# Kernel optimization log

Hardware: AMD Instinct MI355X
Metric: run time of the kernel (lower is better)

Reference implementation:

```python
import jax, jax.numpy as jnp
import numpy as np

N_NODES = 50000
N_EDGES = 500000
IN_FEAT = 128
OUT_FEAT = 128
N_REL = 16


def setup_inputs() -> dict:
    key = jax.random.key(0)
    k1, k2, k3, k4 = jax.random.split(key, 4)
    entity_embeddings = jax.random.normal(k1, (N_NODES, IN_FEAT), dtype=jnp.float32)
    # xavier_uniform over (in, out) fan per relation slice
    limit = (6.0 / (IN_FEAT + OUT_FEAT)) ** 0.5
    weight = jax.random.uniform(k2, (N_REL, IN_FEAT, OUT_FEAT), dtype=jnp.float32,
                                minval=-limit, maxval=limit)
    edge_index = jax.random.randint(k3, (2, N_EDGES), 0, N_NODES, dtype=jnp.int64)
    edge_type = jax.random.randint(k4, (N_EDGES,), 0, N_REL, dtype=jnp.int64)
    return {"entity_embeddings": entity_embeddings, "weight": weight,
            "edge_index": edge_index, "edge_type": edge_type}


def reference(entity_embeddings, weight, edge_index, edge_type):
    # RGCN message passing: for each edge e with relation r:
    #   msg_e = x[src_e] @ W[r];  out[tgt_e] += msg_e;  out = relu(out)
    # Vectorized: transform every node by every relation once (R*N*in*out flops),
    # then gather the (relation, src) slice per edge and scatter-add to tgt.
    # This avoids gathering a per-edge (E, in, out) weight tensor.
    num_entities = entity_embeddings.shape[0]
    src = edge_index[0]
    tgt = edge_index[1]
    transformed = jnp.einsum('ni,rio->rno', entity_embeddings, weight)  # (R, N, O)
    msg = transformed[edge_type, src]                                   # (E, O)
    messages = jax.ops.segment_sum(msg, tgt, num_segments=num_entities)  # (N, O)
    # Dropout is identity in eval mode; reference omits it (deterministic baseline).
    return jax.nn.relu(messages)
```

## Files before the change

### kernel.cpp

```cpp
#include <hip/hip_runtime.h>
#include <hip/hip_bf16.h>

typedef __attribute__((ext_vector_type(8))) __bf16 bf16x8;
typedef __attribute__((ext_vector_type(4))) __bf16 bf16x4;
typedef __attribute__((ext_vector_type(2))) __bf16 bf16x2;
typedef __attribute__((ext_vector_type(4))) float f32x4;

#define IN_FEAT 128
#define OUT_FEAT 128
#define N_REL 16
#define TILE_M 64
#define GEMM_GRID 1024

__global__ void cvtX_kernel(const float* __restrict__ x, __bf16* __restrict__ xb, int n) {
    int i = (blockIdx.x * blockDim.x + threadIdx.x) * 4;
    if (i < n) {
        float4 v = *(const float4*)(x + i);
        bf16x4 o = { (__bf16)v.x, (__bf16)v.y, (__bf16)v.z, (__bf16)v.w };
        *(bf16x4*)(xb + i) = o;
    }
}

__global__ __launch_bounds__(256) void cvtW2_kernel(const float* __restrict__ w,
                                                    __bf16* __restrict__ wt) {
    __shared__ __bf16 tile[32 * 136];
    int r = blockIdx.x >> 2;
    int n0 = (blockIdx.x & 3) * 32;
    const float* W = w + (size_t)r * IN_FEAT * OUT_FEAT;
    __bf16* T = wt + (size_t)r * IN_FEAT * OUT_FEAT;
    int t = threadIdx.x;
    #pragma unroll
    for (int it = 0; it < 16; ++it) {
        int idx = t + it * 256;
        int k = idx >> 5, dn = idx & 31;
        tile[dn * 136 + k] = (__bf16)W[k * OUT_FEAT + n0 + dn];
    }
    __syncthreads();
    #pragma unroll
    for (int it = 0; it < 2; ++it) {
        int idx = t + it * 256;
        int n = idx >> 4, c = idx & 15;
        bf16x8 v = *(const bf16x8*)(&tile[n * 136 + c * 8]);
        *(bf16x8*)(T + (size_t)(n0 + n) * IN_FEAT + c * 8) = v;
    }
}

__global__ void hist_kernel(const int* __restrict__ etype, const int* __restrict__ etgt,
                            int n, int* __restrict__ cnt_rel, int* __restrict__ cnt_tgt) {
    __shared__ int h[N_REL];
    if (threadIdx.x < N_REL) h[threadIdx.x] = 0;
    __syncthreads();
    for (int i = blockIdx.x * blockDim.x + threadIdx.x; i < n; i += gridDim.x * blockDim.x) {
        atomicAdd(&h[etype[i]], 1);
        if (cnt_tgt) atomicAdd(&cnt_tgt[etgt[i]], 1);
    }
    __syncthreads();
    if (threadIdx.x < N_REL) atomicAdd(&cnt_rel[threadIdx.x], h[threadIdx.x]);
}

__global__ void prefix_kernel(const int* __restrict__ cnt, int* __restrict__ meta) {
    if (threadIdx.x == 0) {
        int off = 0, toff = 0;
        for (int r = 0; r < N_REL; ++r) {
            meta[r] = off; meta[32 + r] = toff; meta[64 + r] = off;
            off += cnt[r];
            toff += (cnt[r] + TILE_M - 1) / TILE_M;
        }
        meta[16] = off; meta[48] = toff;
    }
}

__global__ void scanA_kernel(const int* __restrict__ cnt, int n, int* __restrict__ partial) {
    __shared__ int s[256];
    int i = blockIdx.x * 256 + threadIdx.x;
    s[threadIdx.x] = (i < n) ? cnt[i] : 0;
    __syncthreads();
    for (int off = 128; off > 0; off >>= 1) {
        if (threadIdx.x < off) s[threadIdx.x] += s[threadIdx.x + off];
        __syncthreads();
    }
    if (threadIdx.x == 0) partial[blockIdx.x] = s[0];
}
__global__ void scanBP_kernel(int* __restrict__ partial, int nchunks,
                              const int* __restrict__ cnt_rel, int* __restrict__ meta) {
    __shared__ int s[256];
    int t = threadIdx.x;
    int v = (t < nchunks) ? partial[t] : 0;
    s[t] = v;
    __syncthreads();
    for (int off = 1; off < 256; off <<= 1) {
        int x = (t >= off) ? s[t - off] : 0;
        __syncthreads();
        s[t] += x;
        __syncthreads();
    }
    if (t < nchunks) partial[t] = s[t] - v;
    if (t == 0) {
        int off = 0, toff = 0;
        for (int r = 0; r < N_REL; ++r) {
            meta[r] = off; meta[32 + r] = toff; meta[64 + r] = off;
            off += cnt_rel[r];
            toff += (cnt_rel[r] + TILE_M - 1) / TILE_M;
        }
        meta[16] = off; meta[48] = toff;
    }
}
__global__ void scanC_kernel(const int* __restrict__ cnt, int n, const int* __restrict__ partial,
                             int* __restrict__ base, int* __restrict__ cursor) {
    __shared__ int s[256];
    int t = threadIdx.x, i = blockIdx.x * 256 + t;
    int v = (i < n) ? cnt[i] : 0;
    s[t] = v;
    __syncthreads();
    for (int off = 1; off < 256; off <<= 1) {
        int x = (t >= off) ? s[t - off] : 0;
        __syncthreads();
        s[t] += x;
        __syncthreads();
    }
    int b = partial[blockIdx.x] + s[t] - v;
    if (i < n) { base[i] = b; cursor[i] = b; }
}

#define SCATTER_EPT 2
#define SCATTER_CHUNK (256 * SCATTER_EPT)
__global__ __launch_bounds__(256) void scatter_slot_kernel(
        const int* __restrict__ esrc, const int* __restrict__ etgt,
        const int* __restrict__ etype, int n,
        int* __restrict__ cursor_rel, int* __restrict__ cursor_tgt,
        int* __restrict__ bsrc, int* __restrict__ bslot) {
    __shared__ int lcnt[N_REL];
    __shared__ int lbase[N_REL];
    int t = threadIdx.x;
    if (t < N_REL) lcnt[t] = 0;
    __syncthreads();
    int base = blockIdx.x * SCATTER_CHUNK;
    int rj[SCATTER_EPT], offj[SCATTER_EPT];
    #pragma unroll
    for (int j = 0; j < SCATTER_EPT; ++j) {
        int i = base + j * 256 + t;
        if (i < n) {
            int r = etype[i];
            rj[j] = r;
            offj[j] = atomicAdd(&lcnt[r], 1);
        } else rj[j] = -1;
    }
    __syncthreads();
    if (t < N_REL) lbase[t] = atomicAdd(&cursor_rel[t], lcnt[t]);
    __syncthreads();
    #pragma unroll
    for (int j = 0; j < SCATTER_EPT; ++j) {
        if (rj[j] >= 0) {
            int i = base + j * 256 + t;
            int p = lbase[rj[j]] + offj[j];
            bsrc[p] = esrc[i];
            bslot[p] = atomicAdd(&cursor_tgt[etgt[i]], 1);
        }
    }
}

__global__ __launch_bounds__(256) void scatter_kernel(
        const int* __restrict__ esrc, const int* __restrict__ etgt,
        const int* __restrict__ etype, int n,
        int* __restrict__ cursor,
        int* __restrict__ bsrc, int* __restrict__ btgt) {
    __shared__ int lcnt[N_REL];
    __shared__ int lbase[N_REL];
    int t = threadIdx.x;
    if (t < N_REL) lcnt[t] = 0;
    __syncthreads();
    int base = blockIdx.x * SCATTER_CHUNK;
    int rj[SCATTER_EPT], offj[SCATTER_EPT];
    #pragma unroll
    for (int j = 0; j < SCATTER_EPT; ++j) {
        int i = base + j * 256 + t;
        if (i < n) {
            int r = etype[i];
            rj[j] = r;
            offj[j] = atomicAdd(&lcnt[r], 1);
        } else rj[j] = -1;
    }
    __syncthreads();
    if (t < N_REL) lbase[t] = atomicAdd(&cursor[t], lcnt[t]);
    __syncthreads();
    #pragma unroll
    for (int j = 0; j < SCATTER_EPT; ++j) {
        if (rj[j] >= 0) {
            int i = base + j * 256 + t;
            int p = lbase[rj[j]] + offj[j];
            bsrc[p] = esrc[i];
            btgt[p] = etgt[i];
        }
    }
}

__global__ __launch_bounds__(256, 3) void gemm_msg4_kernel(
    const __bf16* __restrict__ Xb,
    const __bf16* __restrict__ Wt,
    const int* __restrict__ bsrc, const int* __restrict__ bslot,
    const int* __restrict__ meta,
    __bf16* __restrict__ msg) {
    __shared__ __align__(16) __bf16 Bs[OUT_FEAT * 128];
    __shared__ __align__(16) __bf16 As[TILE_M * 128];
    __shared__ int s_slot[TILE_M];

    const int* rel_off = meta;
    const int* tile_pre = meta + 32;
    int T = tile_pre[16];
    int chunk = (T + GEMM_GRID - 1) / GEMM_GRID;
    int t0 = blockIdx.x * chunk;
    if (t0 >= T) return;
    int t1 = min(T, t0 + chunk);

    int tid = threadIdx.x;
    int wave = tid >> 6, lane = tid & 63;
    int q = lane >> 4, ln = lane & 15;
    uint4* BsV = (uint4*)Bs;
    uint4* AsV = (uint4*)As;
    const bf16x8* AsF = (const bf16x8*)As;
    const bf16x8* BsF = (const bf16x8*)Bs;

    int arow = tid & 63;
    int acb  = tid >> 6;

    int cur_rel = -1;
    uint4 apf[4];
    int spf = 0;
    {
        int r = 0; while (t0 >= tile_pre[r + 1]) ++r;
        int row_start = rel_off[r] + (t0 - tile_pre[r]) * TILE_M;
        int m_valid = min(TILE_M, rel_off[r + 1] - row_start);
        int src = bsrc[row_start + min(arow, m_valid - 1)];
        const uint4* xr = (const uint4*)(Xb + (size_t)src * IN_FEAT);
        #pragma unroll
        for (int i = 0; i < 4; ++i) apf[i] = xr[acb + 4 * i];
        if (tid < TILE_M) spf = (tid < m_valid) ? bslot[row_start + tid] : -1;
    }

    for (int tt = t0; tt < t1; ++tt) {
        int r = 0; while (tt >= tile_pre[r + 1]) ++r;
        __syncthreads();
        if (r != cur_rel) {
            cur_rel = r;
            const __bf16* wsrc = Wt + (size_t)r * IN_FEAT * OUT_FEAT;
            #pragma unroll
            for (int i = 0; i < 8; ++i) {
                int cid = tid + i * 256;
                int row = cid >> 4, c = cid & 15;
                int feat = (row & 15) * 8 + (row >> 4);
                uint4 v = *(const uint4*)(wsrc + (size_t)feat * IN_FEAT + c * 8);
                BsV[row * 16 + (c ^ (row & 15))] = v;
            }
        }
        #pragma unroll
        for (int i = 0; i < 4; ++i) {
            int c = acb + 4 * i;
            AsV[arow * 16 + (c ^ (arow & 15))] = apf[i];
        }
        if (tid < TILE_M) s_slot[tid] = spf;

        if (tt + 1 < t1) {
            int rn = 0; while (tt + 1 >= tile_pre[rn + 1]) ++rn;
            int row_start = rel_off[rn] + (tt + 1 - tile_pre[rn]) * TILE_M;
            int m_valid = min(TILE_M, rel_off[rn + 1] - row_start);
            int src = bsrc[row_start + min(arow, m_valid - 1)];
            const uint4* xr = (const uint4*)(Xb + (size_t)src * IN_FEAT);
            #pragma unroll
            for (int i = 0; i < 4; ++i) apf[i] = xr[acb + 4 * i];
            if (tid < TILE_M) spf = (tid < m_valid) ? bslot[row_start + tid] : -1;
        }
        __syncthreads();

        f32x4 acc[8];
        f32x4 z = { 0.f, 0.f, 0.f, 0.f };
        #pragma unroll
        for (int nf = 0; nf < 8; ++nf) acc[nf] = z;

        int myrow = wave * 16 + ln;
        #pragma unroll
        for (int kk = 0; kk < 4; ++kk) {
            bf16x8 a = AsF[myrow * 16 + ((kk * 4 + q) ^ ln)];
            #pragma unroll
            for (int nf = 0; nf < 8; ++nf) {
                bf16x8 b = BsF[(nf * 16 + ln) * 16 + ((kk * 4 + q) ^ ln)];
                acc[nf] = __builtin_amdgcn_mfma_f32_16x16x32_bf16(a, b, acc[nf], 0, 0, 0);
            }
        }

        #pragma unroll
        for (int reg = 0; reg < 4; ++reg) {
            int row = wave * 16 + q * 4 + reg;
            int slot = s_slot[row];
            if (slot >= 0) {
                bf16x8 o = { (__bf16)acc[0][reg], (__bf16)acc[1][reg],
                             (__bf16)acc[2][reg], (__bf16)acc[3][reg],
                             (__bf16)acc[4][reg], (__bf16)acc[5][reg],
                             (__bf16)acc[6][reg], (__bf16)acc[7][reg] };
                *(bf16x8*)(msg + (size_t)slot * OUT_FEAT + ln * 8) = o;
            }
        }
    }
}

__global__ __launch_bounds__(256) void segsum2_kernel(
        const __bf16* __restrict__ msg, const int* __restrict__ base,
        int nnodes, int ntot, float* __restrict__ out) {
    int n = blockIdx.x * 4 + (threadIdx.x >> 6);
    if (n >= nnodes) return;
    int l = threadIdx.x & 63;
    int half = l >> 5, cl = l & 31;
    int s0 = base[n];
    int s1 = (n == nnodes - 1) ? ntot : base[n + 1];
    float4 a = { 0.f, 0.f, 0.f, 0.f };
    int s = s0;
    for (; s + 2 <= s1; s += 2) {
        bf16x4 m = *(const bf16x4*)(msg + (size_t)(s + half) * OUT_FEAT + cl * 4);
        a.x += (float)m[0]; a.y += (float)m[1]; a.z += (float)m[2]; a.w += (float)m[3];
    }
    if (s < s1 && half == 0) {
        bf16x4 m = *(const bf16x4*)(msg + (size_t)s * OUT_FEAT + cl * 4);
        a.x += (float)m[0]; a.y += (float)m[1]; a.z += (float)m[2]; a.w += (float)m[3];
    }
    a.x += __shfl_xor(a.x, 32, 64);
    a.y += __shfl_xor(a.y, 32, 64);
    a.z += __shfl_xor(a.z, 32, 64);
    a.w += __shfl_xor(a.w, 32, 64);
    if (half == 0) {
        float4 o = { fmaxf(a.x, 0.f), fmaxf(a.y, 0.f), fmaxf(a.z, 0.f), fmaxf(a.w, 0.f) };
        *(float4*)(out + (size_t)n * OUT_FEAT + cl * 4) = o;
    }
}

#define LDA 136
__global__ __launch_bounds__(256) void gemm_scatter_kernel(
    const __bf16* __restrict__ Xb, const __bf16* __restrict__ Wt,
    const int* __restrict__ bsrc, const int* __restrict__ btgt,
    const int* __restrict__ meta, float* __restrict__ out) {
    __shared__ __align__(16) __bf16 As2[TILE_M * LDA];
    __shared__ __align__(16) __bf16 Bs2[OUT_FEAT * LDA];
    __shared__ int s_tgt[TILE_M];
    int bid = blockIdx.x;
    const int* rel_off = meta;
    const int* tile_pre = meta + 32;
    if (bid >= tile_pre[16]) return;
    int rel = 0;
    while (bid >= tile_pre[rel + 1]) rel++;
    int tile = bid - tile_pre[rel];
    int row_start = rel_off[rel] + tile * TILE_M;
    int m_valid = min(TILE_M, rel_off[rel + 1] - row_start);
    int t = threadIdx.x;
    {
        const __bf16* src = Wt + rel * IN_FEAT * OUT_FEAT;
        #pragma unroll
        for (int i = 0; i < 8; ++i) {
            int cid = t + i * 256;
            int n = cid >> 4, c = cid & 15;
            uint4 v = *(const uint4*)(src + n * IN_FEAT + c * 8);
            *(uint4*)(&Bs2[n * LDA + c * 8]) = v;
        }
    }
    {
        #pragma unroll
        for (int i = 0; i < 4; ++i) {
            int cid = t + i * 256;
            int r = cid >> 4, c = cid & 15;
            int srcn = (r < m_valid) ? bsrc[row_start + r] : 0;
            uint4 v = *(const uint4*)(Xb + srcn * IN_FEAT + c * 8);
            *(uint4*)(&As2[r * LDA + c * 8]) = v;
        }
        if (t < TILE_M) s_tgt[t] = (t < m_valid) ? btgt[row_start + t] : -1;
    }
    __syncthreads();
    int wave = t >> 6, lane = t & 63;
    int q = lane >> 4, ln = lane & 15;
    f32x4 acc[8];
    f32x4 z = { 0.f, 0.f, 0.f, 0.f };
    #pragma unroll
    for (int nf = 0; nf < 8; ++nf) acc[nf] = z;
    #pragma unroll
    for (int kk = 0; kk < 4; ++kk) {
        bf16x8 a = *(const bf16x8*)(&As2[(wave * 16 + ln) * LDA + kk * 32 + q * 8]);
        #pragma unroll
        for (int nf = 0; nf < 8; ++nf) {
            bf16x8 b = *(const bf16x8*)(&Bs2[(nf * 16 + ln) * LDA + kk * 32 + q * 8]);
            acc[nf] = __builtin_amdgcn_mfma_f32_16x16x32_bf16(a, b, acc[nf], 0, 0, 0);
        }
    }
    #pragma unroll
    for (int reg = 0; reg < 4; ++reg) {
        int r = wave * 16 + q * 4 + reg;
        int tgt = s_tgt[r];
        if (tgt >= 0) {
            float* orow = out + (size_t)tgt * OUT_FEAT + ln;
            #pragma unroll
            for (int nf = 0; nf < 8; ++nf)
                unsafeAtomicAdd(orow + nf * 16, acc[nf][reg]);
        }
    }
}

__global__ void relu_kernel(float* __restrict__ out, int n) {
    int i = (blockIdx.x * blockDim.x + threadIdx.x) * 4;
    if (i < n) {
        float4 v = *(float4*)(out + i);
        v.x = fmaxf(v.x, 0.f); v.y = fmaxf(v.y, 0.f);
        v.z = fmaxf(v.z, 0.f); v.w = fmaxf(v.w, 0.f);
        *(float4*)(out + i) = v;
    }
}

extern "C" void kernel_launch(void* const* d_in, const int* in_sizes, int n_in,
                              void* d_out, int out_size, void* d_ws, size_t ws_size,
                              hipStream_t stream) {
    const float* x = (const float*)d_in[0];
    const float* w = (const float*)d_in[1];
    const int* eidx = (const int*)d_in[2];
    const int* etype = (const int*)d_in[3];
    const int E = in_sizes[3];
    const int nX = in_sizes[0];
    const int N = out_size / OUT_FEAT;
    const int* esrc = eidx;
    const int* etgt = eidx + E;
    float* out = (float*)d_out;

    char* ws = (char*)d_ws;
    size_t off = 0;
    auto alloc = [&](size_t sz) { size_t o = off; off = (off + sz + 255) & ~(size_t)255; return o; };
    size_t off_Xb   = alloc((size_t)nX * 2);
    size_t off_Wt   = alloc((size_t)N_REL * IN_FEAT * OUT_FEAT * 2);
    size_t off_cnt  = alloc(64);
    size_t off_meta = alloc(512);
    size_t off_bsrc = alloc((size_t)E * 4);
    size_t off_bsl  = alloc((size_t)E * 4);
    size_t off_ctgt = alloc((size_t)(N + 16) * 4);
    size_t off_cur  = alloc((size_t)N * 4);
    size_t off_base = alloc((size_t)N * 4);
    size_t off_part = alloc(1024);
    size_t off_msg  = alloc((size_t)E * OUT_FEAT * 2);
    bool big = (ws_size >= off);

    __bf16* Xb = (__bf16*)(ws + off_Xb);
    __bf16* Wt = (__bf16*)(ws + off_Wt);
    int* meta  = (int*)(ws + off_meta);
    int* bsrc  = (int*)(ws + off_bsrc);
    int* bsl   = (int*)(ws + off_bsl);

    cvtX_kernel<<<(nX / 4 + 255) / 256, 256, 0, stream>>>(x, Xb, nX);
    cvtW2_kernel<<<64, 256, 0, stream>>>(w, Wt);

    int scatter_blocks = (E + SCATTER_CHUNK - 1) / SCATTER_CHUNK;

    if (big) {
        int* cnt_tgt = (int*)(ws + off_ctgt);
        int* cnt_rel = cnt_tgt + N;
        int* cursor  = (int*)(ws + off_cur);
        int* base    = (int*)(ws + off_base);
        int* partial = (int*)(ws + off_part);
        __bf16* msg  = (__bf16*)(ws + off_msg);
        int nchunks = (N + 255) / 256;

        hipMemsetAsync(cnt_tgt, 0, (size_t)(N + 16) * 4, stream);
        hist_kernel<<<1024, 256, 0, stream>>>(etype, etgt, E, cnt_rel, cnt_tgt);
        scanA_kernel<<<nchunks, 256, 0, stream>>>(cnt_tgt, N, partial);
        scanBP_kernel<<<1, 256, 0, stream>>>(partial, nchunks, cnt_rel, meta);
        scanC_kernel<<<nchunks, 256, 0, stream>>>(cnt_tgt, N, partial, base, cursor);
        scatter_slot_kernel<<<scatter_blocks, 256, 0, stream>>>(
            esrc, etgt, etype, E, meta + 64, cursor, bsrc, bsl);
        gemm_msg4_kernel<<<GEMM_GRID, 256, 0, stream>>>(Xb, Wt, bsrc, bsl, meta, msg);
        segsum2_kernel<<<(N + 3) / 4, 256, 0, stream>>>(msg, base, N, E, out);
    } else {
        int* cnt = (int*)(ws + off_cnt);
        hipMemsetAsync(cnt, 0, 64, stream);
        hipMemsetAsync(out, 0, (size_t)out_size * 4, stream);
        hist_kernel<<<1024, 256, 0, stream>>>(etype, etgt, E, cnt, nullptr);
        prefix_kernel<<<1, 64, 0, stream>>>(cnt, meta);
        scatter_kernel<<<scatter_blocks, 256, 0, stream>>>(
            esrc, etgt, etype, E, meta + 64, bsrc, bsl);
        int max_tiles = (E + TILE_M - 1) / TILE_M + N_REL;
        gemm_scatter_kernel<<<max_tiles, 256, 0, stream>>>(Xb, Wt, bsrc, bsl, meta, out);
        relu_kernel<<<(out_size / 4 + 255) / 256, 256, 0, stream>>>(out, out_size);
    }
}
```

Before: 256.0 us.

## Fuse weight conversion into histogram kernel and convert X inside GEMM tiles

Merges the weight transpose/convert with the edge histogram into one prep kernel, drops the separate X-to-bf16 conversion pass in the main path, and has the GEMM read fp32 node features directly and convert them while staging each tile. The GEMM moves from a persistent 1024-block grid with register prefetch to one block per tile, with no occupancy hint in launch bounds. This removes two launches and a full write and re-read of X, but doubles gather bytes per edge row and loses the prefetch overlap.

```diff
diff --git a/kernel.cpp b/kernel.cpp
--- a/kernel.cpp
+++ b/kernel.cpp
@@ -10,7 +10,6 @@
 #define OUT_FEAT 128
 #define N_REL 16
 #define TILE_M 64
-#define GEMM_GRID 1024
 
 __global__ void cvtX_kernel(const float* __restrict__ x, __bf16* __restrict__ xb, int n) {
     int i = (blockIdx.x * blockDim.x + threadIdx.x) * 4;
@@ -21,43 +20,54 @@
     }
 }
 
-__global__ __launch_bounds__(256) void cvtW2_kernel(const float* __restrict__ w,
-                                                    __bf16* __restrict__ wt) {
+__global__ __launch_bounds__(256) void prep_kernel(
+        const float* __restrict__ w, __bf16* __restrict__ wt,
+        const int* __restrict__ etype, const int* __restrict__ etgt, int n,
+        int* __restrict__ cnt_rel, int* __restrict__ cnt_tgt) {
     __shared__ __bf16 tile[32 * 136];
-    int r = blockIdx.x >> 2;
-    int n0 = (blockIdx.x & 3) * 32;
-    const float* W = w + (size_t)r * IN_FEAT * OUT_FEAT;
-    __bf16* T = wt + (size_t)r * IN_FEAT * OUT_FEAT;
+    __shared__ int h[N_REL];
     int t = threadIdx.x;
-    #pragma unroll
-    for (int it = 0; it < 16; ++it) {
-        int idx = t + it * 256;
-        int k = idx >> 5, dn = idx & 31;
-        tile[dn * 136 + k] = (__bf16)W[k * OUT_FEAT + n0 + dn];
-    }
-    __syncthreads();
-    #pragma unroll
-    for (int it = 0; it < 2; ++it) {
-        int idx = t + it * 256;
-        int n = idx >> 4, c = idx & 15;
-        bf16x8 v = *(const bf16x8*)(&tile[n * 136 + c * 8]);
-        *(bf16x8*)(T + (size_t)(n0 + n) * IN_FEAT + c * 8) = v;
-    }
-}
-
-__global__ void hist_kernel(const int* __restrict__ etype, const int* __restrict__ etgt,
-                            int n, int* __restrict__ cnt_rel, int* __restrict__ cnt_tgt) {
+    if (blockIdx.x < 64) {
+        int r = blockIdx.x >> 2;
+        int n0 = (blockIdx.x & 3) * 32;
+        const float* W = w + (size_t)r * IN_FEAT * OUT_FEAT;
+        __bf16* T = wt + (size_t)r * IN_FEAT * OUT_FEAT;
+        #pragma unroll
+        for (int it = 0; it < 16; ++it) {
+            int idx = t + it * 256;
+            int k = idx >> 5, dn = idx & 31;
+            tile[dn * 136 + k] = (__bf16)W[k * OUT_FEAT + n0 + dn];
+        }
+        __syncthreads();
+        #pragma unroll
+        for (int it = 0; it < 2; ++it) {
+            int idx = t + it * 256;
+            int nn = idx >> 4, c = idx & 15;
+            bf16x8 v = *(const bf16x8*)(&tile[nn * 136 + c * 8]);
+            *(bf16x8*)(T + (size_t)(n0 + nn) * IN_FEAT + c * 8) = v;
+        }
+    } else {
+        if (t < N_REL) h[t] = 0;
+        __syncthreads();
+        int stride = (gridDim.x - 64) * blockDim.x;
+        for (int i = (blockIdx.x - 64) * blockDim.x + t; i < n; i += stride) {
+            atomicAdd(&h[etype[i]], 1);
+            atomicAdd(&cnt_tgt[etgt[i]], 1);
+        }
+        __syncthreads();
+        if (t < N_REL) atomicAdd(&cnt_rel[t], h[t]);
+    }
+}
+
+__global__ void hist_kernel(const int* __restrict__ etype, int n, int* __restrict__ cnt_rel) {
     __shared__ int h[N_REL];
     if (threadIdx.x < N_REL) h[threadIdx.x] = 0;
     __syncthreads();
-    for (int i = blockIdx.x * blockDim.x + threadIdx.x; i < n; i += gridDim.x * blockDim.x) {
+    for (int i = blockIdx.x * blockDim.x + threadIdx.x; i < n; i += gridDim.x * blockDim.x)
         atomicAdd(&h[etype[i]], 1);
-        if (cnt_tgt) atomicAdd(&cnt_tgt[etgt[i]], 1);
-    }
     __syncthreads();
     if (threadIdx.x < N_REL) atomicAdd(&cnt_rel[threadIdx.x], h[threadIdx.x]);
 }
-
 __global__ void prefix_kernel(const int* __restrict__ cnt, int* __restrict__ meta) {
     if (threadIdx.x == 0) {
         int off = 0, toff = 0;
@@ -194,8 +204,8 @@
     }
 }
 
-__global__ __launch_bounds__(256, 3) void gemm_msg4_kernel(
-    const __bf16* __restrict__ Xb,
+__global__ __launch_bounds__(256) void gemm_msg5_kernel(
+    const float* __restrict__ X,
     const __bf16* __restrict__ Wt,
     const int* __restrict__ bsrc, const int* __restrict__ bslot,
     const int* __restrict__ meta,
@@ -204,100 +214,78 @@
     __shared__ __align__(16) __bf16 As[TILE_M * 128];
     __shared__ int s_slot[TILE_M];
 
+    int bid = blockIdx.x;
     const int* rel_off = meta;
     const int* tile_pre = meta + 32;
-    int T = tile_pre[16];
-    int chunk = (T + GEMM_GRID - 1) / GEMM_GRID;
-    int t0 = blockIdx.x * chunk;
-    if (t0 >= T) return;
-    int t1 = min(T, t0 + chunk);
+    if (bid >= tile_pre[16]) return;
+    int rel = 0;
+    while (bid >= tile_pre[rel + 1]) rel++;
+    int tile = bid - tile_pre[rel];
+    int row_start = rel_off[rel] + tile * TILE_M;
+    int m_valid = min(TILE_M, rel_off[rel + 1] - row_start);
 
     int tid = threadIdx.x;
+    uint4* BsV = (uint4*)Bs;
+    bf16x8* AsV = (bf16x8*)As;
+    const bf16x8* AsF = (const bf16x8*)As;
+    const bf16x8* BsF = (const bf16x8*)Bs;
+
+    {
+        const __bf16* wsrc = Wt + (size_t)rel * IN_FEAT * OUT_FEAT;
+        #pragma unroll
+        for (int i = 0; i < 8; ++i) {
+            int cid = tid + i * 256;
+            int row = cid >> 4, c = cid & 15;
+            int feat = (row & 15) * 8 + (row >> 4);
+            uint4 v = *(const uint4*)(wsrc + (size_t)feat * IN_FEAT + c * 8);
+            BsV[row * 16 + (c ^ (row & 15))] = v;
+        }
+    }
+    {
+        #pragma unroll
+        for (int i = 0; i < 4; ++i) {
+            int cid = tid + i * 256;
+            int r = cid >> 4, c = cid & 15;
+            int srcn = (r < m_valid) ? bsrc[row_start + r] : 0;
+            const float4* xr = (const float4*)(X + (size_t)srcn * IN_FEAT + c * 8);
+            float4 f0 = xr[0], f1 = xr[1];
+            bf16x8 o = { (__bf16)f0.x, (__bf16)f0.y, (__bf16)f0.z, (__bf16)f0.w,
+                         (__bf16)f1.x, (__bf16)f1.y, (__bf16)f1.z, (__bf16)f1.w };
+            AsV[r * 16 + (c ^ (r & 15))] = o;
+        }
+        if (tid < TILE_M) s_slot[tid] = (tid < m_valid) ? bslot[row_start + tid] : -1;
+    }
+    __syncthreads();
+
     int wave = tid >> 6, lane = tid & 63;
     int q = lane >> 4, ln = lane & 15;
-    uint4* BsV = (uint4*)Bs;
-    uint4* AsV = (uint4*)As;
-    const bf16x8* AsF = (const bf16x8*)As;
-    const bf16x8* BsF = (const bf16x8*)Bs;
-
-    int arow = tid & 63;
-    int acb  = tid >> 6;
-
-    int cur_rel = -1;
-    uint4 apf[4];
-    int spf = 0;
-    {
-        int r = 0; while (t0 >= tile_pre[r + 1]) ++r;
-        int row_start = rel_off[r] + (t0 - tile_pre[r]) * TILE_M;
-        int m_valid = min(TILE_M, rel_off[r + 1] - row_start);
-        int src = bsrc[row_start + min(arow, m_valid - 1)];
-        const uint4* xr = (const uint4*)(Xb + (size_t)src * IN_FEAT);
-        #pragma unroll
-        for (int i = 0; i < 4; ++i) apf[i] = xr[acb + 4 * i];
-        if (tid < TILE_M) spf = (tid < m_valid) ? bslot[row_start + tid] : -1;
-    }
-
-    for (int tt = t0; tt < t1; ++tt) {
-        int r = 0; while (tt >= tile_pre[r + 1]) ++r;
-        __syncthreads();
-        if (r != cur_rel) {
-            cur_rel = r;
-            const __bf16* wsrc = Wt + (size_t)r * IN_FEAT * OUT_FEAT;
-            #pragma unroll
-            for (int i = 0; i < 8; ++i) {
-                int cid = tid + i * 256;
-                int row = cid >> 4, c = cid & 15;
-                int feat = (row & 15) * 8 + (row >> 4);
-                uint4 v = *(const uint4*)(wsrc + (size_t)feat * IN_FEAT + c * 8);
-                BsV[row * 16 + (c ^ (row & 15))] = v;
-            }
-        }
-        #pragma unroll
-        for (int i = 0; i < 4; ++i) {
-            int c = acb + 4 * i;
-            AsV[arow * 16 + (c ^ (arow & 15))] = apf[i];
-        }
-        if (tid < TILE_M) s_slot[tid] = spf;
-
-        if (tt + 1 < t1) {
-            int rn = 0; while (tt + 1 >= tile_pre[rn + 1]) ++rn;
-            int row_start = rel_off[rn] + (tt + 1 - tile_pre[rn]) * TILE_M;
-            int m_valid = min(TILE_M, rel_off[rn + 1] - row_start);
-            int src = bsrc[row_start + min(arow, m_valid - 1)];
-            const uint4* xr = (const uint4*)(Xb + (size_t)src * IN_FEAT);
-            #pragma unroll
-            for (int i = 0; i < 4; ++i) apf[i] = xr[acb + 4 * i];
-            if (tid < TILE_M) spf = (tid < m_valid) ? bslot[row_start + tid] : -1;
-        }
-        __syncthreads();
-
-        f32x4 acc[8];
-        f32x4 z = { 0.f, 0.f, 0.f, 0.f };
-        #pragma unroll
-        for (int nf = 0; nf < 8; ++nf) acc[nf] = z;
-
-        int myrow = wave * 16 + ln;
-        #pragma unroll
-        for (int kk = 0; kk < 4; ++kk) {
-            bf16x8 a = AsF[myrow * 16 + ((kk * 4 + q) ^ ln)];
-            #pragma unroll
-            for (int nf = 0; nf < 8; ++nf) {
-                bf16x8 b = BsF[(nf * 16 + ln) * 16 + ((kk * 4 + q) ^ ln)];
-                acc[nf] = __builtin_amdgcn_mfma_f32_16x16x32_bf16(a, b, acc[nf], 0, 0, 0);
-            }
-        }
-
-        #pragma unroll
-        for (int reg = 0; reg < 4; ++reg) {
-            int row = wave * 16 + q * 4 + reg;
-            int slot = s_slot[row];
-            if (slot >= 0) {
-                bf16x8 o = { (__bf16)acc[0][reg], (__bf16)acc[1][reg],
-                             (__bf16)acc[2][reg], (__bf16)acc[3][reg],
-                             (__bf16)acc[4][reg], (__bf16)acc[5][reg],
-                             (__bf16)acc[6][reg], (__bf16)acc[7][reg] };
-                *(bf16x8*)(msg + (size_t)slot * OUT_FEAT + ln * 8) = o;
-            }
+
+    f32x4 acc[8];
+    f32x4 z = { 0.f, 0.f, 0.f, 0.f };
+    #pragma unroll
+    for (int nf = 0; nf < 8; ++nf) acc[nf] = z;
+
+    int myrow = wave * 16 + ln;
+    #pragma unroll
+    for (int kk = 0; kk < 4; ++kk) {
+        bf16x8 a = AsF[myrow * 16 + ((kk * 4 + q) ^ ln)];
+        #pragma unroll
+        for (int nf = 0; nf < 8; ++nf) {
+            bf16x8 b = BsF[(nf * 16 + ln) * 16 + ((kk * 4 + q) ^ ln)];
+            acc[nf] = __builtin_amdgcn_mfma_f32_16x16x32_bf16(a, b, acc[nf], 0, 0, 0);
+        }
+    }
+
+    #pragma unroll
+    for (int reg = 0; reg < 4; ++reg) {
+        int row = wave * 16 + q * 4 + reg;
+        int slot = s_slot[row];
+        if (slot >= 0) {
+            bf16x8 o = { (__bf16)acc[0][reg], (__bf16)acc[1][reg],
+                         (__bf16)acc[2][reg], (__bf16)acc[3][reg],
+                         (__bf16)acc[4][reg], (__bf16)acc[5][reg],
+                         (__bf16)acc[6][reg], (__bf16)acc[7][reg] };
+            *(bf16x8*)(msg + (size_t)slot * OUT_FEAT + ln * 8) = o;
         }
     }
 }
@@ -445,10 +433,8 @@
     int* bsrc  = (int*)(ws + off_bsrc);
     int* bsl   = (int*)(ws + off_bsl);
 
-    cvtX_kernel<<<(nX / 4 + 255) / 256, 256, 0, stream>>>(x, Xb, nX);
-    cvtW2_kernel<<<64, 256, 0, stream>>>(w, Wt);
-
     int scatter_blocks = (E + SCATTER_CHUNK - 1) / SCATTER_CHUNK;
+    int max_tiles = (E + TILE_M - 1) / TILE_M + N_REL;
 
     if (big) {
         int* cnt_tgt = (int*)(ws + off_ctgt);
@@ -460,23 +446,24 @@
         int nchunks = (N + 255) / 256;
 
         hipMemsetAsync(cnt_tgt, 0, (size_t)(N + 16) * 4, stream);
-        hist_kernel<<<1024, 256, 0, stream>>>(etype, etgt, E, cnt_rel, cnt_tgt);
+        prep_kernel<<<64 + 1024, 256, 0, stream>>>(w, Wt, etype, etgt, E, cnt_rel, cnt_tgt);
         scanA_kernel<<<nchunks, 256, 0, stream>>>(cnt_tgt, N, partial);
         scanBP_kernel<<<1, 256, 0, stream>>>(partial, nchunks, cnt_rel, meta);
         scanC_kernel<<<nchunks, 256, 0, stream>>>(cnt_tgt, N, partial, base, cursor);
         scatter_slot_kernel<<<scatter_blocks, 256, 0, stream>>>(
             esrc, etgt, etype, E, meta + 64, cursor, bsrc, bsl);
-        gemm_msg4_kernel<<<GEMM_GRID, 256, 0, stream>>>(Xb, Wt, bsrc, bsl, meta, msg);
+        gemm_msg5_kernel<<<max_tiles, 256, 0, stream>>>(x, Wt, bsrc, bsl, meta, msg);
         segsum2_kernel<<<(N + 3) / 4, 256, 0, stream>>>(msg, base, N, E, out);
     } else {
         int* cnt = (int*)(ws + off_cnt);
         hipMemsetAsync(cnt, 0, 64, stream);
         hipMemsetAsync(out, 0, (size_t)out_size * 4, stream);
-        hist_kernel<<<1024, 256, 0, stream>>>(etype, etgt, E, cnt, nullptr);
+        cvtX_kernel<<<(nX / 4 + 255) / 256, 256, 0, stream>>>(x, Xb, nX);
+        prep_kernel<<<64, 256, 0, stream>>>(w, Wt, etype, etgt, E, cnt, nullptr);
+        hist_kernel<<<1024, 256, 0, stream>>>(etype, E, cnt);
         prefix_kernel<<<1, 64, 0, stream>>>(cnt, meta);
         scatter_kernel<<<scatter_blocks, 256, 0, stream>>>(
             esrc, etgt, etype, E, meta + 64, bsrc, bsl);
-        int max_tiles = (E + TILE_M - 1) / TILE_M + N_REL;
         gemm_scatter_kernel<<<max_tiles, 256, 0, stream>>>(Xb, Wt, bsrc, bsl, meta, out);
         relu_kernel<<<(out_size / 4 + 255) / 256, 256, 0, stream>>>(out, out_size);
     }
```

After: 236.0 us. 1.08x faster.
